# Kernel tuning notes

Measured on AMD Instinct MI355X. Metric: run time of the kernel, lower is better.

The kernel has to match this reference:

```python
import jax, jax.numpy as jnp
import numpy as np

B, NPG = 128, 512            # graphs, nodes per graph (batch is contiguous & uniform)
N = B * NPG                  # 65536 nodes
DEG = 8
E = N * DEG                  # 524288 edges
F_IN, NHID = 128, 64
H, C = 3, NHID               # GAT heads, out channels per head
HC = H * C                   # 192
NCLS = 10
RATIO = 0.5
NEG_SLOPE = 0.2


def setup_inputs() -> dict:
    key = jax.random.key(0)
    ks = jax.random.split(key, 24)
    x = jax.random.normal(ks[0], (N, F_IN), jnp.float32)
    # edges constrained within each graph (graphs are contiguous blocks of NPG nodes)
    offs = jnp.repeat(jnp.arange(B, dtype=jnp.int32) * NPG, NPG * DEG)
    src = jax.random.randint(ks[1], (E,), 0, NPG, dtype=jnp.int32) + offs
    dst = jax.random.randint(ks[2], (E,), 0, NPG, dtype=jnp.int32) + offs
    edge_index = jnp.stack([src, dst], axis=0)
    edge_attr = jax.random.normal(ks[3], (E, 2), jnp.float32)
    batch = jnp.repeat(jnp.arange(B, dtype=jnp.int32), NPG)

    def lin(k, o, i):
        return jax.random.normal(k, (o, i), jnp.float32) / np.float32(np.sqrt(i))

    return {
        "x": x, "edge_index": edge_index, "edge_attr": edge_attr, "batch": batch,
        # lin: num_features -> nhid//2
        "W_lin": lin(ks[4], NHID // 2, F_IN), "b_lin": jnp.zeros((NHID // 2,), jnp.float32),
        # GATConv(nhid//2 -> nhid, heads=3, edge_dim=2)
        "W_src": lin(ks[5], HC, NHID // 2),
        "att_src": jax.random.normal(ks[6], (H, C), jnp.float32) / np.float32(np.sqrt(C)),
        "att_dst": jax.random.normal(ks[7], (H, C), jnp.float32) / np.float32(np.sqrt(C)),
        "W_edge": lin(ks[8], HC, 2),
        "att_edge": jax.random.normal(ks[9], (H, C), jnp.float32) / np.float32(np.sqrt(C)),
        "b_gat": jnp.zeros((HC,), jnp.float32),
        # SAGPool score layer: GCNConv(nhid*3 -> 1)
        "W_gcn": lin(ks[10], 1, HC), "b_gcn": jnp.zeros((1,), jnp.float32),
        # classifier MLP
        "W1": lin(ks[11], NHID, 2 * HC), "b1": jnp.zeros((NHID,), jnp.float32),
        "W2": lin(ks[12], NHID // 2, NHID), "b2": jnp.zeros((NHID // 2,), jnp.float32),
        "W3": lin(ks[13], NCLS, NHID // 2), "b3": jnp.zeros((NCLS,), jnp.float32),
    }


def reference(x, edge_index, edge_attr, batch,
              W_lin, b_lin, W_src, att_src, att_dst, W_edge, att_edge, b_gat,
              W_gcn, b_gcn, W1, b1, W2, b2, W3, b3):
    src, dst = edge_index[0], edge_index[1]

    # ---- lin + ELU -------------------------------------------------------
    h = jax.nn.elu(x @ W_lin.T + b_lin)                       # [N, nhid//2]

    # ---- GATConv(heads=3, edge_dim=2), add_self_loops fill_value='mean' --
    loop = jnp.arange(N, dtype=src.dtype)
    cnt = jax.ops.segment_sum(jnp.ones((E,), h.dtype), dst, num_segments=N)
    loop_attr = jax.ops.segment_sum(edge_attr, dst, num_segments=N) / jnp.maximum(cnt, 1.0)[:, None]
    s_full = jnp.concatenate([src, loop])
    d_full = jnp.concatenate([dst, loop])
    ea_full = jnp.concatenate([edge_attr, loop_attr], axis=0)  # [E+N, 2]

    xp = (h @ W_src.T).reshape(N, H, C)                        # projected per-head feats
    a_src = (xp * att_src).sum(-1)                             # [N, H]
    a_dst = (xp * att_dst).sum(-1)                             # [N, H]
    ef = (ea_full @ W_edge.T).reshape(-1, H, C)
    a_edge = (ef * att_edge).sum(-1)                           # [E+N, H]

    alpha = jax.nn.leaky_relu(a_src[s_full] + a_dst[d_full] + a_edge, NEG_SLOPE)
    m = jax.ops.segment_max(alpha, d_full, num_segments=N)     # scatter-softmax over dst
    ealpha = jnp.exp(alpha - m[d_full])
    denom = jax.ops.segment_sum(ealpha, d_full, num_segments=N)
    alpha = ealpha / (denom[d_full] + 1e-16)                   # [E+N, H]

    out = jax.ops.segment_sum(alpha[:, :, None] * xp[s_full], d_full, num_segments=N)
    x1 = jax.nn.relu(out.reshape(N, HC) + b_gat)               # [N, 192]

    # ---- SAGPool: GCNConv score + per-graph top-k (mask form) ------------
    xw = x1 @ W_gcn.T                                          # [N, 1]
    deg = jax.ops.segment_sum(jnp.ones((E,), x1.dtype), dst, num_segments=N) + 1.0
    dinv = jax.lax.rsqrt(deg)
    agg = jax.ops.segment_sum((dinv[src] * dinv[dst])[:, None] * xw[src], dst, num_segments=N)
    score = (agg + (dinv ** 2)[:, None] * xw + b_gcn)[:, 0]    # [N]

    k = int(np.ceil(RATIO * NPG))                              # nodes kept per graph
    s2 = score.reshape(B, NPG)
    rank = jnp.argsort(jnp.argsort(-s2, axis=1), axis=1)
    mask = rank < k                                            # [B, NPG] top-k selection

    xs = (x1 * jnp.tanh(score)[:, None]).reshape(B, NPG, HC)
    gmp = jnp.max(jnp.where(mask[:, :, None], xs, -jnp.inf), axis=1)   # [B, 192]
    gap = jnp.sum(jnp.where(mask[:, :, None], xs, 0.0), axis=1) / k    # [B, 192]
    r = jnp.concatenate([gmp, gap], axis=1)                    # [B, 384]

    # ---- classifier MLP (dropout is identity in eval) ---------------------
    r = jax.nn.relu(r @ W1.T + b1)
    r = jax.nn.relu(r @ W2.T + b2)
    return jax.nn.log_softmax(r @ W3.T + b3, axis=-1)          # [B, num_classes]
```

## Files before the change

kernel.cpp:

```cpp
#include <hip/hip_runtime.h>
#include <hip/hip_bf16.h>
#include <math.h>

#define NN   65536
#define EE   524288
#define BB   128
#define NPGC 512
#define HCC  192
#define KSEL 256
#define NEG  0.2f
#define PSEG 8
#define SEGN (NPGC / PSEG)
#define MAXD 40
#define SLOTS ((size_t)NN * MAXD)
#define EPG   4096

__global__ __launch_bounds__(256) void k_prep(
    const float* __restrict__ W_lin, const float* __restrict__ W_src,
    const float* __restrict__ W_edge, const float* __restrict__ att_edge,
    float* __restrict__ WlT, float* __restrict__ WsT,
    float* __restrict__ acoef) {
    int gid = blockIdx.x * 256 + threadIdx.x;
    if (gid < 4096) {
        int j = gid >> 7, k = gid & 127;
        WlT[k * 32 + j] = W_lin[gid];
    }
    if (gid < 6144) {
        int j = gid >> 5, k = gid & 31;
        WsT[k * 192 + j] = W_src[gid];
    }
    if (blockIdx.x == 24) {
        __shared__ float red[6];
        int t = threadIdx.x;
        if (t < 6) red[t] = 0.f;
        __syncthreads();
        if (t < 192) {
            float ae = att_edge[t];
            int h = t >> 6;
            atomicAdd(&red[h],     W_edge[2 * t]     * ae);
            atomicAdd(&red[3 + h], W_edge[2 * t + 1] * ae);
        }
        __syncthreads();
        if (t < 6) acoef[t] = red[t];
    }
}

__device__ __forceinline__ int nodeblock_base(int bx) {
    int xcd = bx & 7, j = bx >> 3;
    int g = xcd + 8 * (j >> 1);
    return g * NPGC + (j & 1) * 256;
}

__global__ __launch_bounds__(256) void k_h(
    const float* __restrict__ x, const float* __restrict__ WlT,
    const float* __restrict__ b_lin, float* __restrict__ hbuf) {
    __shared__ float Wl[128 * 16];
    int t = threadIdx.x;
    int half = blockIdx.y;
#pragma unroll
    for (int i = 0; i < 8; ++i) {
        int idx = t + i * 256;
        int k = idx >> 4, jj = idx & 15;
        Wl[idx] = WlT[k * 32 + half * 16 + jj];
    }
    __syncthreads();
    int n = nodeblock_base(blockIdx.x) + t;
    const float4* xr = (const float4*)(x + (size_t)n * 128);
    float acc[16];
#pragma unroll
    for (int j = 0; j < 16; ++j) acc[j] = b_lin[half * 16 + j];
#pragma unroll 4
    for (int q = 0; q < 32; ++q) {
        float4 a = xr[q];
        const float* w = &Wl[(q * 4) * 16];
#pragma unroll
        for (int j = 0; j < 16; ++j) {
            acc[j] += a.x * w[j] + a.y * w[16 + j] +
                      a.z * w[32 + j] + a.w * w[48 + j];
        }
    }
#pragma unroll
    for (int j = 0; j < 16; ++j)
        acc[j] = acc[j] > 0.f ? acc[j] : expm1f(acc[j]);
    float4* dst = (float4*)(hbuf + (size_t)n * 32 + half * 16);
#pragma unroll
    for (int q = 0; q < 4; ++q)
        dst[q] = make_float4(acc[4 * q], acc[4 * q + 1],
                             acc[4 * q + 2], acc[4 * q + 3]);
}

__global__ __launch_bounds__(256) void k_xp(
    const float* __restrict__ hbuf, const float* __restrict__ WsT,
    const float* __restrict__ att_src, const float* __restrict__ att_dst,
    float* __restrict__ xp, float* __restrict__ ap_s, float* __restrict__ ap_d) {
    int n = nodeblock_base(blockIdx.x) + threadIdx.x;
    int h = blockIdx.y;
    int ch = blockIdx.z;
    const float4* hr = (const float4*)(hbuf + (size_t)n * 32);
    float acc[32];
#pragma unroll
    for (int c = 0; c < 32; ++c) acc[c] = 0.f;
#pragma unroll
    for (int q = 0; q < 8; ++q) {
        float4 hv = hr[q];
        const float* w = WsT + (q * 4) * 192 + h * 64 + ch * 32;
#pragma unroll
        for (int c = 0; c < 32; ++c) {
            acc[c] += hv.x * w[c] + hv.y * w[192 + c] +
                      hv.z * w[384 + c] + hv.w * w[576 + c];
        }
    }
    float as = 0.f, ad = 0.f;
    const float* ats = att_src + h * 64 + ch * 32;
    const float* atd = att_dst + h * 64 + ch * 32;
#pragma unroll
    for (int c = 0; c < 32; ++c) {
        as += acc[c] * ats[c];
        ad += acc[c] * atd[c];
    }
    ap_s[((size_t)n * 3 + h) * 2 + ch] = as;
    ap_d[((size_t)n * 3 + h) * 2 + ch] = ad;
    float4* dst = (float4*)(xp + (size_t)n * HCC + h * 64 + ch * 32);
#pragma unroll
    for (int q = 0; q < 8; ++q)
        dst[q] = make_float4(acc[4 * q], acc[4 * q + 1],
                             acc[4 * q + 2], acc[4 * q + 3]);
}

__global__ __launch_bounds__(1024) void k_edges(
    const int* __restrict__ ei, const float* __restrict__ ea,
    const float* __restrict__ ap_s, const float* __restrict__ ap_d,
    const float* __restrict__ acoef,
    int* __restrict__ fill, float* __restrict__ la,
    float4* __restrict__ slotA) {
    __shared__ int   s_cnt[NPGC], s_pos[NPGC];
    __shared__ float s_la[NPGC * 2];
    __shared__ float s_as[NPGC * 3], s_ad[NPGC * 3];
    int b = blockIdx.x, t = threadIdx.x;
    int g = (b & 7) + 8 * (b >> 3);
    int nbase = g * NPGC;
    int ebase = g * EPG;
    if (t < NPGC) { s_cnt[t] = 0; s_pos[t] = 0; }
    s_la[t] = 0.f;
    const float2* aps2 = (const float2*)ap_s;
    const float2* apd2 = (const float2*)ap_d;
    for (int i = t; i < NPGC * 3; i += 1024) {
        float2 ps = aps2[(size_t)nbase * 3 + i];
        float2 pd = apd2[(size_t)nbase * 3 + i];
        s_as[i] = ps.x + ps.y;
        s_ad[i] = pd.x + pd.y;
    }
    __syncthreads();
#pragma unroll
    for (int k = 0; k < 4; ++k) {
        int e = ebase + t + k * 1024;
        int dl = ei[EE + e] & (NPGC - 1);
        atomicAdd(&s_cnt[dl], 1);
        atomicAdd(&s_la[2 * dl],     ea[2 * e]);
        atomicAdd(&s_la[2 * dl + 1], ea[2 * e + 1]);
    }
    __syncthreads();
    if (t < NPGC) {
        fill[nbase + t] = s_cnt[t];
        ((float2*)la)[nbase + t] = make_float2(s_la[2 * t], s_la[2 * t + 1]);
    }
    float ac[6];
#pragma unroll
    for (int h = 0; h < 6; ++h) ac[h] = acoef[h];
#pragma unroll
    for (int k = 0; k < 4; ++k) {
        int e = ebase + t + k * 1024;
        int s = ei[e], d = ei[EE + e];
        int sl = s & (NPGC - 1), dl = d & (NPGC - 1);
        float e0 = ea[2 * e], e1 = ea[2 * e + 1];
        float v[3];
#pragma unroll
        for (int h = 0; h < 3; ++h) {
            float a = s_as[sl * 3 + h] + s_ad[dl * 3 + h] +
                      e0 * ac[h] + e1 * ac[3 + h];
            v[h] = a >= 0.f ? a : NEG * a;
        }
        int pos = atomicAdd(&s_pos[dl], 1);
        if (pos < MAXD - 1)
            slotA[(size_t)d * MAXD + 1 + pos] =
                make_float4(v[0], v[1], v[2], __int_as_float(s));
    }
}

__global__ __launch_bounds__(256) void k_agg(
    const int* __restrict__ fill, const float4* __restrict__ slotA,
    const float* __restrict__ la,
    const float* __restrict__ ap_s, const float* __restrict__ ap_d,
    const float* __restrict__ acoef, const float* __restrict__ xp,
    const float* __restrict__ b_gat, const float* __restrict__ W_gcn,
    float* __restrict__ x1, float* __restrict__ xwd, float* __restrict__ dinv) {
    __shared__ float4 wsl[4][64];
    int wave = threadIdx.x >> 6, lane = threadIdx.x & 63;
    int b = blockIdx.x;
    int xcd = b & 7, j = b >> 3;
    int g = (j >> 7) * 8 + xcd;
    int n = g * NPGC + (j & 127) * 4 + wave;

    int ctrue = fill[n];
    int cnt = ctrue < (MAXD - 1) ? ctrue : (MAXD - 1);
    int tot = cnt + 1;

    float4 ent;
    if (lane == 0) {
        float inv = 1.f / fmaxf((float)ctrue, 1.f);
        float l0 = la[2 * n] * inv, l1 = la[2 * n + 1] * inv;
        const float2* aps2 = (const float2*)ap_s;
        const float2* apd2 = (const float2*)ap_d;
        float e[3];
#pragma unroll
        for (int h = 0; h < 3; ++h) {
            float2 ps = aps2[(size_t)n * 3 + h];
            float2 pd = apd2[(size_t)n * 3 + h];
            float v = (ps.x + ps.y) + (pd.x + pd.y) +
                      l0 * acoef[h] + l1 * acoef[3 + h];
            v = v >= 0.f ? v : NEG * v;
            e[h] = __expf(v);
        }
        ent = make_float4(e[0], e[1], e[2], __int_as_float(n));
    } else if (lane <= cnt) {
        float4 pk = slotA[(size_t)n * MAXD + lane];
        ent = make_float4(__expf(pk.x), __expf(pk.y), __expf(pk.z), pk.w);
    } else {
        ent = make_float4(0.f, 0.f, 0.f, 0.f);
    }
    wsl[wave][lane] = ent;

    int head = lane >> 4;
    bool act = lane < 48;
    const float4* xp4 = (const float4*)xp;
    float ax = 0.f, ay = 0.f, az = 0.f, aw = 0.f, den = 0.f;
    int s = 0;
    for (; s + 3 < tot; s += 4) {
        float4 eA = wsl[wave][s],     eB = wsl[wave][s + 1];
        float4 eC = wsl[wave][s + 2], eD = wsl[wave][s + 3];
        float wA = head == 0 ? eA.x : (head == 1 ? eA.y : eA.z);
        float wB = head == 0 ? eB.x : (head == 1 ? eB.y : eB.z);
        float wC = head == 0 ? eC.x : (head == 1 ? eC.y : eC.z);
        float wD = head == 0 ? eD.x : (head == 1 ? eD.y : eD.z);
        den += (wA + wB) + (wC + wD);
        if (act) {
            float4 vA = xp4[(size_t)__float_as_int(eA.w) * 48 + lane];
            float4 vB = xp4[(size_t)__float_as_int(eB.w) * 48 + lane];
            float4 vC = xp4[(size_t)__float_as_int(eC.w) * 48 + lane];
            float4 vD = xp4[(size_t)__float_as_int(eD.w) * 48 + lane];
            ax += wA * vA.x + wB * vB.x + wC * vC.x + wD * vD.x;
            ay += wA * vA.y + wB * vB.y + wC * vC.y + wD * vD.y;
            az += wA * vA.z + wB * vB.z + wC * vC.z + wD * vD.z;
            aw += wA * vA.w + wB * vB.w + wC * vC.w + wD * vD.w;
        }
    }
    for (; s < tot; ++s) {
        float4 eA = wsl[wave][s];
        float wA = head == 0 ? eA.x : (head == 1 ? eA.y : eA.z);
        den += wA;
        if (act) {
            float4 vA = xp4[(size_t)__float_as_int(eA.w) * 48 + lane];
            ax += wA * vA.x; ay += wA * vA.y; az += wA * vA.z; aw += wA * vA.w;
        }
    }
    float p = 0.f;
    if (act) {
        float id = 1.f / (den + 1e-16f);
        float4 bg = ((const float4*)b_gat)[lane];
        float4 v;
        v.x = fmaxf(ax * id + bg.x, 0.f);
        v.y = fmaxf(ay * id + bg.y, 0.f);
        v.z = fmaxf(az * id + bg.z, 0.f);
        v.w = fmaxf(aw * id + bg.w, 0.f);
        ((float4*)x1)[(size_t)n * 48 + lane] = v;
        float4 wg = ((const float4*)W_gcn)[lane];
        p = v.x * wg.x + v.y * wg.y + v.z * wg.z + v.w * wg.w;
    }
#pragma unroll
    for (int msk = 32; msk > 0; msk >>= 1) p += __shfl_xor(p, msk, 64);
    if (lane == 0) {
        float dv = rsqrtf((float)ctrue + 1.f);
        xwd[n] = p * dv;
        dinv[n] = dv;
    }
}

__global__ __launch_bounds__(256) void k_score(
    const int* __restrict__ fill, const float4* __restrict__ slotA,
    const float* __restrict__ xwd, const float* __restrict__ dinv,
    const float* __restrict__ b_gcn, float* __restrict__ score) {
    int wave = threadIdx.x >> 6, lane = threadIdx.x & 63;
    int b = blockIdx.x;
    int xcd = b & 7, j = b >> 3;
    int g = (j >> 7) * 8 + xcd;
    int n = g * NPGC + (j & 127) * 4 + wave;

    int ctrue = fill[n];
    int cnt = ctrue < (MAXD - 1) ? ctrue : (MAXD - 1);
    float acc = 0.f;
    if (lane == 0) {
        acc = xwd[n];
    } else if (lane <= cnt) {
        int src = __float_as_int(
            ((const float*)slotA)[((size_t)n * MAXD + lane) * 4 + 3]);
        acc = xwd[src];
    }
#pragma unroll
    for (int msk = 32; msk > 0; msk >>= 1) acc += __shfl_xor(acc, msk, 64);
    if (lane == 0) score[n] = b_gcn[0] + dinv[n] * acc;
}

__global__ __launch_bounds__(192) void k_poolrank(
    const float* __restrict__ score, const float* __restrict__ x1,
    float* __restrict__ pmax, float* __restrict__ psum) {
    __shared__ float sc[NPGC];
    __shared__ float ts_s[SEGN];
    __shared__ int sel_s[SEGN];
    int b = blockIdx.x;
    int xcd = b & 7, gslot = (b >> 3) & 15, seg = b >> 7;
    int g = gslot * 8 + xcd;
    int t = threadIdx.x;
    int gbase = g * NPGC;
    for (int i = t; i < NPGC; i += 192) sc[i] = score[gbase + i];
    __syncthreads();
    if (t < SEGN) {
        int iloc = seg * SEGN + t;
        float si = sc[iloc];
        int rank = 0;
        for (int j = 0; j < NPGC; ++j) {
            float sj = sc[j];
            rank += (sj > si) || (sj == si && j < iloc);
        }
        sel_s[t] = (rank < KSEL) ? 1 : 0;
        ts_s[t] = tanhf(si);
    }
    __syncthreads();
    int nb = gbase + seg * SEGN;
    float mx = -1e30f, sm = 0.f;
    for (int i = 0; i < SEGN; ++i) {
        if (sel_s[i]) {
            float v = x1[(size_t)(nb + i) * HCC + t] * ts_s[i];
            mx = fmaxf(mx, v);
            sm += v;
        }
    }
    size_t pb = (size_t)(g * PSEG + seg) * HCC + t;
    pmax[pb] = mx;
    psum[pb] = sm;
}

__global__ __launch_bounds__(384) void k_mlp(
    const float* __restrict__ pmax, const float* __restrict__ psum,
    const float* __restrict__ W1, const float* __restrict__ b1,
    const float* __restrict__ W2, const float* __restrict__ b2,
    const float* __restrict__ W3, const float* __restrict__ b3,
    float* __restrict__ out) {
    __shared__ float rs[384], part[384], h1[64], h2[32], lg[10], mls;
    int g = blockIdx.x, t = threadIdx.x;
    if (t < HCC) {
        float mx = -1e30f, sm = 0.f;
#pragma unroll
        for (int s = 0; s < PSEG; ++s) {
            mx = fmaxf(mx, pmax[(size_t)(g * PSEG + s) * HCC + t]);
            sm += psum[(size_t)(g * PSEG + s) * HCC + t];
        }
        rs[t] = mx;
        rs[HCC + t] = sm * (1.f / (float)KSEL);
    }
    __syncthreads();
    {
        int o = t / 6, sl = t - o * 6;
        const float* wr = W1 + o * 384 + sl * 64;
        const float* rr = rs + sl * 64;
        float s = 0.f;
#pragma unroll 8
        for (int k = 0; k < 64; ++k) s += rr[k] * wr[k];
        part[t] = s;
    }
    __syncthreads();
    if (t < 64) {
        float s = b1[t];
#pragma unroll
        for (int j = 0; j < 6; ++j) s += part[t * 6 + j];
        h1[t] = fmaxf(s, 0.f);
    }
    __syncthreads();
    if (t < 256) {
        int o = t >> 3, sl = t & 7;
        const float* wr = W2 + o * 64 + sl * 8;
        const float* hr = h1 + sl * 8;
        float s = 0.f;
#pragma unroll
        for (int k = 0; k < 8; ++k) s += hr[k] * wr[k];
        part[t] = s;
    }
    __syncthreads();
    if (t < 32) {
        float s = b2[t];
#pragma unroll
        for (int j = 0; j < 8; ++j) s += part[t * 8 + j];
        h2[t] = fmaxf(s, 0.f);
    }
    __syncthreads();
    if (t < 10) {
        float s = b3[t];
        for (int k = 0; k < 32; ++k) s += h2[k] * W3[t * 32 + k];
        lg[t] = s;
    }
    __syncthreads();
    if (t == 0) {
        float mx = lg[0];
        for (int j = 1; j < 10; ++j) mx = fmaxf(mx, lg[j]);
        float se = 0.f;
        for (int j = 0; j < 10; ++j) se += expf(lg[j] - mx);
        mls = mx + logf(se);
    }
    __syncthreads();
    if (t < 10) out[g * 10 + t] = lg[t] - mls;
}

extern "C" void kernel_launch(void* const* d_in, const int* in_sizes, int n_in,
                              void* d_out, int out_size, void* d_ws, size_t ws_size,
                              hipStream_t stream) {
    const float* x        = (const float*)d_in[0];
    const int*   ei       = (const int*)d_in[1];
    const float* ea       = (const float*)d_in[2];
    const float* W_lin    = (const float*)d_in[4];
    const float* b_lin    = (const float*)d_in[5];
    const float* W_src    = (const float*)d_in[6];
    const float* att_src  = (const float*)d_in[7];
    const float* att_dst  = (const float*)d_in[8];
    const float* W_edge   = (const float*)d_in[9];
    const float* att_edge = (const float*)d_in[10];
    const float* b_gat    = (const float*)d_in[11];
    const float* W_gcn    = (const float*)d_in[12];
    const float* b_gcn    = (const float*)d_in[13];
    const float* W1 = (const float*)d_in[14]; const float* b1 = (const float*)d_in[15];
    const float* W2 = (const float*)d_in[16]; const float* b2 = (const float*)d_in[17];
    const float* W3 = (const float*)d_in[18]; const float* b3 = (const float*)d_in[19];
    float* out = (float*)d_out;

    char* ws = (char*)d_ws;
    size_t off = 0;
    auto alloc = [&](size_t bytes) {
        size_t r = off;
        off += (bytes + 255) & ~(size_t)255;
        return r;
    };
    float* xp      = (float*)(ws + alloc((size_t)NN * HCC * 4));
    float* x1      = (float*)(ws + alloc((size_t)NN * HCC * 4));
    float* hbuf    = (float*)(ws + alloc((size_t)NN * 32 * 4));
    int*   fill    = (int*)(ws + alloc((size_t)NN * 4));
    float* la      = (float*)(ws + alloc((size_t)NN * 2 * 4));
    float* ap_s    = (float*)(ws + alloc((size_t)NN * 6 * 4));
    float* ap_d    = (float*)(ws + alloc((size_t)NN * 6 * 4));
    float4* slotA  = (float4*)(ws + alloc(SLOTS * 16));
    float* xwd     = (float*)(ws + alloc((size_t)NN * 4));
    float* dinv    = (float*)(ws + alloc((size_t)NN * 4));
    float* score   = (float*)(ws + alloc((size_t)NN * 4));
    float* acoef   = (float*)(ws + alloc(8 * 4));
    float* WlT     = (float*)(ws + alloc(4096 * 4));
    float* WsT     = (float*)(ws + alloc(6144 * 4));
    float* pmax    = (float*)(ws + alloc((size_t)BB * PSEG * HCC * 4));
    float* psum    = (float*)(ws + alloc((size_t)BB * PSEG * HCC * 4));

    k_prep<<<25, 256, 0, stream>>>(W_lin, W_src, W_edge, att_edge,
                                   WlT, WsT, acoef);
    k_h<<<dim3(256, 2), 256, 0, stream>>>(x, WlT, b_lin, hbuf);
    k_xp<<<dim3(256, 3, 2), 256, 0, stream>>>(hbuf, WsT, att_src, att_dst,
                                              xp, ap_s, ap_d);
    k_edges<<<BB, 1024, 0, stream>>>(ei, ea, ap_s, ap_d, acoef,
                                     fill, la, slotA);
    k_agg<<<NN / 4, 256, 0, stream>>>(fill, slotA, la, ap_s, ap_d,
                                      acoef, xp, b_gat, W_gcn, x1, xwd, dinv);
    k_score<<<NN / 4, 256, 0, stream>>>(fill, slotA, xwd, dinv, b_gcn, score);
    k_poolrank<<<BB * PSEG, 192, 0, stream>>>(score, x1, pmax, psum);
    k_mlp<<<BB, 384, 0, stream>>>(pmax, psum, W1, b1, W2, b2, W3, b3, out);
}
```

Before: 276.3 us.

## Drop weight prep kernel and compute self-loop attention entry inside edge kernel

Removes the k_prep launch. The weight transposes now happen inside k_h and k_xp (k_xp stages W_src through shared memory), and the edge-attention coefficients are reduced per block in k_edges. The self-loop logit, which uses mean edge attributes, moves from k_agg into k_edges and is written to slot 0 of slotA. This removes the la buffer and lets k_agg and k_score treat every slot uniformly. ap_s/ap_d switch to a head-major planar layout, so k_xp's writes become coalesced. In exchange, every block repeats the small weight reductions.

```diff
diff --git a/kernel.cpp b/kernel.cpp
--- a/kernel.cpp
+++ b/kernel.cpp
@@ -15,36 +15,6 @@
 #define SLOTS ((size_t)NN * MAXD)
 #define EPG   4096
 
-__global__ __launch_bounds__(256) void k_prep(
-    const float* __restrict__ W_lin, const float* __restrict__ W_src,
-    const float* __restrict__ W_edge, const float* __restrict__ att_edge,
-    float* __restrict__ WlT, float* __restrict__ WsT,
-    float* __restrict__ acoef) {
-    int gid = blockIdx.x * 256 + threadIdx.x;
-    if (gid < 4096) {
-        int j = gid >> 7, k = gid & 127;
-        WlT[k * 32 + j] = W_lin[gid];
-    }
-    if (gid < 6144) {
-        int j = gid >> 5, k = gid & 31;
-        WsT[k * 192 + j] = W_src[gid];
-    }
-    if (blockIdx.x == 24) {
-        __shared__ float red[6];
-        int t = threadIdx.x;
-        if (t < 6) red[t] = 0.f;
-        __syncthreads();
-        if (t < 192) {
-            float ae = att_edge[t];
-            int h = t >> 6;
-            atomicAdd(&red[h],     W_edge[2 * t]     * ae);
-            atomicAdd(&red[3 + h], W_edge[2 * t + 1] * ae);
-        }
-        __syncthreads();
-        if (t < 6) acoef[t] = red[t];
-    }
-}
-
 __device__ __forceinline__ int nodeblock_base(int bx) {
     int xcd = bx & 7, j = bx >> 3;
     int g = xcd + 8 * (j >> 1);
@@ -52,7 +22,7 @@
 }
 
 __global__ __launch_bounds__(256) void k_h(
-    const float* __restrict__ x, const float* __restrict__ WlT,
+    const float* __restrict__ x, const float* __restrict__ W_lin,
     const float* __restrict__ b_lin, float* __restrict__ hbuf) {
     __shared__ float Wl[128 * 16];
     int t = threadIdx.x;
@@ -61,7 +31,7 @@
     for (int i = 0; i < 8; ++i) {
         int idx = t + i * 256;
         int k = idx >> 4, jj = idx & 15;
-        Wl[idx] = WlT[k * 32 + half * 16 + jj];
+        Wl[idx] = W_lin[(half * 16 + jj) * 128 + k];
     }
     __syncthreads();
     int n = nodeblock_base(blockIdx.x) + t;
@@ -90,12 +60,24 @@
 }
 
 __global__ __launch_bounds__(256) void k_xp(
-    const float* __restrict__ hbuf, const float* __restrict__ WsT,
+    const float* __restrict__ hbuf, const float* __restrict__ W_src,
     const float* __restrict__ att_src, const float* __restrict__ att_dst,
     float* __restrict__ xp, float* __restrict__ ap_s, float* __restrict__ ap_d) {
-    int n = nodeblock_base(blockIdx.x) + threadIdx.x;
+    __shared__ float Ws[32 * 33];
+    int t = threadIdx.x;
     int h = blockIdx.y;
     int ch = blockIdx.z;
+    {
+        int rowbase = (h * 64 + ch * 32) * 32;
+#pragma unroll
+        for (int i = 0; i < 4; ++i) {
+            int idx = t + i * 256;
+            int r = idx >> 5, k = idx & 31;
+            Ws[k * 33 + r] = W_src[rowbase + idx];
+        }
+    }
+    __syncthreads();
+    int n = nodeblock_base(blockIdx.x) + t;
     const float4* hr = (const float4*)(hbuf + (size_t)n * 32);
     float acc[32];
 #pragma unroll
@@ -103,11 +85,11 @@
 #pragma unroll
     for (int q = 0; q < 8; ++q) {
         float4 hv = hr[q];
-        const float* w = WsT + (q * 4) * 192 + h * 64 + ch * 32;
+        const float* w = &Ws[(q * 4) * 33];
 #pragma unroll
         for (int c = 0; c < 32; ++c) {
-            acc[c] += hv.x * w[c] + hv.y * w[192 + c] +
-                      hv.z * w[384 + c] + hv.w * w[576 + c];
+            acc[c] += hv.x * w[c] + hv.y * w[33 + c] +
+                      hv.z * w[66 + c] + hv.w * w[99 + c];
         }
     }
     float as = 0.f, ad = 0.f;
@@ -118,8 +100,8 @@
         as += acc[c] * ats[c];
         ad += acc[c] * atd[c];
     }
-    ap_s[((size_t)n * 3 + h) * 2 + ch] = as;
-    ap_d[((size_t)n * 3 + h) * 2 + ch] = ad;
+    ap_s[(size_t)(ch * 3 + h) * NN + n] = as;
+    ap_d[(size_t)(ch * 3 + h) * NN + n] = ad;
     float4* dst = (float4*)(xp + (size_t)n * HCC + h * 64 + ch * 32);
 #pragma unroll
     for (int q = 0; q < 8; ++q)
@@ -130,27 +112,33 @@
 __global__ __launch_bounds__(1024) void k_edges(
     const int* __restrict__ ei, const float* __restrict__ ea,
     const float* __restrict__ ap_s, const float* __restrict__ ap_d,
-    const float* __restrict__ acoef,
-    int* __restrict__ fill, float* __restrict__ la,
-    float4* __restrict__ slotA) {
+    const float* __restrict__ W_edge, const float* __restrict__ att_edge,
+    int* __restrict__ fill, float4* __restrict__ slotA) {
     __shared__ int   s_cnt[NPGC], s_pos[NPGC];
     __shared__ float s_la[NPGC * 2];
     __shared__ float s_as[NPGC * 3], s_ad[NPGC * 3];
+    __shared__ float s_ac[6];
     int b = blockIdx.x, t = threadIdx.x;
     int g = (b & 7) + 8 * (b >> 3);
     int nbase = g * NPGC;
     int ebase = g * EPG;
     if (t < NPGC) { s_cnt[t] = 0; s_pos[t] = 0; }
     s_la[t] = 0.f;
-    const float2* aps2 = (const float2*)ap_s;
-    const float2* apd2 = (const float2*)ap_d;
+    if (t < 6) s_ac[t] = 0.f;
     for (int i = t; i < NPGC * 3; i += 1024) {
-        float2 ps = aps2[(size_t)nbase * 3 + i];
-        float2 pd = apd2[(size_t)nbase * 3 + i];
-        s_as[i] = ps.x + ps.y;
-        s_ad[i] = pd.x + pd.y;
-    }
-    __syncthreads();
+        int h = i >> 9, nl = i & (NPGC - 1);
+        s_as[nl * 3 + h] = ap_s[(size_t)h * NN + nbase + nl] +
+                           ap_s[(size_t)(3 + h) * NN + nbase + nl];
+        s_ad[nl * 3 + h] = ap_d[(size_t)h * NN + nbase + nl] +
+                           ap_d[(size_t)(3 + h) * NN + nbase + nl];
+    }
+    __syncthreads();
+    if (t < 192) {
+        float ae = att_edge[t];
+        int h = t >> 6;
+        atomicAdd(&s_ac[h],     W_edge[2 * t]     * ae);
+        atomicAdd(&s_ac[3 + h], W_edge[2 * t + 1] * ae);
+    }
 #pragma unroll
     for (int k = 0; k < 4; ++k) {
         int e = ebase + t + k * 1024;
@@ -160,13 +148,25 @@
         atomicAdd(&s_la[2 * dl + 1], ea[2 * e + 1]);
     }
     __syncthreads();
+    float ac[6];
+#pragma unroll
+    for (int h = 0; h < 6; ++h) ac[h] = s_ac[h];
     if (t < NPGC) {
-        fill[nbase + t] = s_cnt[t];
-        ((float2*)la)[nbase + t] = make_float2(s_la[2 * t], s_la[2 * t + 1]);
-    }
-    float ac[6];
-#pragma unroll
-    for (int h = 0; h < 6; ++h) ac[h] = acoef[h];
+        int cnt = s_cnt[t];
+        int n = nbase + t;
+        fill[n] = cnt;
+        float inv = 1.f / fmaxf((float)cnt, 1.f);
+        float l0 = s_la[2 * t] * inv, l1 = s_la[2 * t + 1] * inv;
+        float v[3];
+#pragma unroll
+        for (int h = 0; h < 3; ++h) {
+            float a = s_as[t * 3 + h] + s_ad[t * 3 + h] +
+                      l0 * ac[h] + l1 * ac[3 + h];
+            v[h] = a >= 0.f ? a : NEG * a;
+        }
+        slotA[(size_t)n * MAXD] = make_float4(v[0], v[1], v[2],
+                                              __int_as_float(n));
+    }
 #pragma unroll
     for (int k = 0; k < 4; ++k) {
         int e = ebase + t + k * 1024;
@@ -189,9 +189,7 @@
 
 __global__ __launch_bounds__(256) void k_agg(
     const int* __restrict__ fill, const float4* __restrict__ slotA,
-    const float* __restrict__ la,
-    const float* __restrict__ ap_s, const float* __restrict__ ap_d,
-    const float* __restrict__ acoef, const float* __restrict__ xp,
+    const float* __restrict__ xp,
     const float* __restrict__ b_gat, const float* __restrict__ W_gcn,
     float* __restrict__ x1, float* __restrict__ xwd, float* __restrict__ dinv) {
     __shared__ float4 wsl[4][64];
@@ -205,28 +203,10 @@
     int cnt = ctrue < (MAXD - 1) ? ctrue : (MAXD - 1);
     int tot = cnt + 1;
 
-    float4 ent;
-    if (lane == 0) {
-        float inv = 1.f / fmaxf((float)ctrue, 1.f);
-        float l0 = la[2 * n] * inv, l1 = la[2 * n + 1] * inv;
-        const float2* aps2 = (const float2*)ap_s;
-        const float2* apd2 = (const float2*)ap_d;
-        float e[3];
-#pragma unroll
-        for (int h = 0; h < 3; ++h) {
-            float2 ps = aps2[(size_t)n * 3 + h];
-            float2 pd = apd2[(size_t)n * 3 + h];
-            float v = (ps.x + ps.y) + (pd.x + pd.y) +
-                      l0 * acoef[h] + l1 * acoef[3 + h];
-            v = v >= 0.f ? v : NEG * v;
-            e[h] = __expf(v);
-        }
-        ent = make_float4(e[0], e[1], e[2], __int_as_float(n));
-    } else if (lane <= cnt) {
+    float4 ent = make_float4(0.f, 0.f, 0.f, 0.f);
+    if (lane < tot) {
         float4 pk = slotA[(size_t)n * MAXD + lane];
         ent = make_float4(__expf(pk.x), __expf(pk.y), __expf(pk.z), pk.w);
-    } else {
-        ent = make_float4(0.f, 0.f, 0.f, 0.f);
     }
     wsl[wave][lane] = ent;
 
@@ -298,9 +278,7 @@
     int ctrue = fill[n];
     int cnt = ctrue < (MAXD - 1) ? ctrue : (MAXD - 1);
     float acc = 0.f;
-    if (lane == 0) {
-        acc = xwd[n];
-    } else if (lane <= cnt) {
+    if (lane <= cnt) {
         int src = __float_as_int(
             ((const float*)slotA)[((size_t)n * MAXD + lane) * 4 + 3]);
         acc = xwd[src];
@@ -451,28 +429,22 @@
     float* x1      = (float*)(ws + alloc((size_t)NN * HCC * 4));
     float* hbuf    = (float*)(ws + alloc((size_t)NN * 32 * 4));
     int*   fill    = (int*)(ws + alloc((size_t)NN * 4));
-    float* la      = (float*)(ws + alloc((size_t)NN * 2 * 4));
     float* ap_s    = (float*)(ws + alloc((size_t)NN * 6 * 4));
     float* ap_d    = (float*)(ws + alloc((size_t)NN * 6 * 4));
     float4* slotA  = (float4*)(ws + alloc(SLOTS * 16));
     float* xwd     = (float*)(ws + alloc((size_t)NN * 4));
     float* dinv    = (float*)(ws + alloc((size_t)NN * 4));
     float* score   = (float*)(ws + alloc((size_t)NN * 4));
-    float* acoef   = (float*)(ws + alloc(8 * 4));
-    float* WlT     = (float*)(ws + alloc(4096 * 4));
-    float* WsT     = (float*)(ws + alloc(6144 * 4));
     float* pmax    = (float*)(ws + alloc((size_t)BB * PSEG * HCC * 4));
     float* psum    = (float*)(ws + alloc((size_t)BB * PSEG * HCC * 4));
 
-    k_prep<<<25, 256, 0, stream>>>(W_lin, W_src, W_edge, att_edge,
-                                   WlT, WsT, acoef);
-    k_h<<<dim3(256, 2), 256, 0, stream>>>(x, WlT, b_lin, hbuf);
-    k_xp<<<dim3(256, 3, 2), 256, 0, stream>>>(hbuf, WsT, att_src, att_dst,
+    k_h<<<dim3(256, 2), 256, 0, stream>>>(x, W_lin, b_lin, hbuf);
+    k_xp<<<dim3(256, 3, 2), 256, 0, stream>>>(hbuf, W_src, att_src, att_dst,
                                               xp, ap_s, ap_d);
-    k_edges<<<BB, 1024, 0, stream>>>(ei, ea, ap_s, ap_d, acoef,
-                                     fill, la, slotA);
-    k_agg<<<NN / 4, 256, 0, stream>>>(fill, slotA, la, ap_s, ap_d,
-                                      acoef, xp, b_gat, W_gcn, x1, xwd, dinv);
+    k_edges<<<BB, 1024, 0, stream>>>(ei, ea, ap_s, ap_d, W_edge, att_edge,
+                                     fill, slotA);
+    k_agg<<<NN / 4, 256, 0, stream>>>(fill, slotA, xp, b_gat, W_gcn,
+                                      x1, xwd, dinv);
     k_score<<<NN / 4, 256, 0, stream>>>(fill, slotA, xwd, dinv, b_gcn, score);
     k_poolrank<<<BB * PSEG, 192, 0, stream>>>(score, x1, pmax, psum);
     k_mlp<<<BB, 384, 0, stream>>>(pmax, psum, W1, b1, W2, b2, W3, b3, out);
```

Result: faster. 264.4 us (-4.3%).
